# Optimization experiments

Measured on AMD Instinct MI355X. Metric: run time of the kernel, lower is better.

## Reference

```python
import jax, jax.numpy as jnp
import numpy as np

IMG, P, D, E, TOPK, H = 224, 14, 512, 10, 2, 8
NP = (IMG // P) ** 2  # 256 patches
PD = P * P            # 196
HID = 256             # expert hidden (hardcoded in source)


def _moe_layer(x, Wip, bip, Wqkv, bqkv, Wo, bo, Wg, bg, W1, b1, W2, b2):
    # input projection (input_dim == adjusted_dim == 512 here)
    h = x @ Wip + bip                                  # [b, s, d]
    b, s, d = h.shape
    hd = d // H
    # torch nn.MultiheadAttention with batch_first=False receives [b, s, d]
    # untransposed -> seq axis is the BATCH axis (l,m below), batch axis is
    # the patch axis (n). Faithfully reproduced.
    qkv = h @ Wqkv + bqkv                              # [b, s, 3d]
    q, k, v = jnp.split(qkv, 3, axis=-1)
    q = q.reshape(b, s, H, hd)
    k = k.reshape(b, s, H, hd)
    v = v.reshape(b, s, H, hd)
    scores = jnp.einsum('lnhd,mnhd->nhlm', q, k) / np.sqrt(hd)
    attn = jax.nn.softmax(scores, axis=-1)             # [s, H, b, b]
    o = jnp.einsum('nhlm,mnhd->lnhd', attn, v).reshape(b, s, d)
    o = o @ Wo + bo                                    # [b, s, d]
    # gating + top-k dispatch
    probs = jax.nn.softmax(o @ Wg + bg, axis=-1)       # [b, s, E]
    topv, topi = jax.lax.top_k(probs, TOPK)
    topv = topv / jnp.sum(topv, axis=-1, keepdims=True)
    # combine weights per (token, expert): [b, s, E]
    w = jnp.sum(jax.nn.one_hot(topi, E, dtype=o.dtype) * topv[..., None], axis=2)
    # expert MLPs (dense over experts, weighted combine == masked scatter-add)
    h1 = jax.nn.relu(jnp.einsum('bsd,edh->bseh', o, W1) + b1)   # [b, s, E, HID]
    out = jnp.einsum('bseh,eho,bse->bso', h1, W2, w) \
        + jnp.einsum('bse,eo->bso', w, b2)
    return out


def _patchify(x):
    # x: [b, 1, IMG, IMG] -> [b, NP, PD]  (unfold/unfold/permute in source)
    b = x.shape[0]
    n = IMG // P
    x = x.reshape(b, n, P, n, P)
    x = x.transpose(0, 1, 3, 2, 4)
    return x.reshape(b, n * n, PD)


def _moe_params(key, prefix):
    ks = jax.random.split(key, 12)
    g = lambda k, shape: jax.random.normal(k, shape, jnp.float32) * 0.02
    return {
        prefix + 'Wip': g(ks[0], (D, D)),   prefix + 'bip': jnp.zeros((D,), jnp.float32),
        prefix + 'Wqkv': g(ks[1], (D, 3 * D)), prefix + 'bqkv': jnp.zeros((3 * D,), jnp.float32),
        prefix + 'Wo': g(ks[2], (D, D)),    prefix + 'bo': jnp.zeros((D,), jnp.float32),
        prefix + 'Wg': g(ks[3], (D, E)),    prefix + 'bg': jnp.zeros((E,), jnp.float32),
        prefix + 'W1': g(ks[4], (E, D, HID)), prefix + 'b1': jnp.zeros((E, HID), jnp.float32),
        prefix + 'W2': g(ks[5], (E, HID, D)), prefix + 'b2': jnp.zeros((E, D), jnp.float32),
    }


def setup_inputs() -> dict:
    key = jax.random.key(0)
    ks = jax.random.split(key, 8)
    g = lambda k, shape: jax.random.normal(k, shape, jnp.float32) * 0.02
    inp = {'x': jax.random.normal(ks[0], (64, 1, IMG, IMG), jnp.float32)}
    inp['pos_emb'] = g(ks[1], (1, NP, D))
    inp['Wp'] = g(ks[2], (PD, D))
    inp['bp'] = jnp.zeros((D,), jnp.float32)
    inp.update(_moe_params(ks[3], 'm1_'))
    inp.update(_moe_params(ks[4], 'm2_'))
    inp['Wv'] = g(ks[5], (D, D))
    inp['bv'] = jnp.zeros((D,), jnp.float32)
    inp['Wc'] = g(ks[6], (D, D))
    inp['bc'] = jnp.zeros((D,), jnp.float32)
    return inp


def reference(x, pos_emb, Wp, bp,
              m1_Wip, m1_bip, m1_Wqkv, m1_bqkv, m1_Wo, m1_bo, m1_Wg, m1_bg,
              m1_W1, m1_b1, m1_W2, m1_b2,
              m2_Wip, m2_bip, m2_Wqkv, m2_bqkv, m2_Wo, m2_bo, m2_Wg, m2_bg,
              m2_W1, m2_b1, m2_W2, m2_b2,
              Wv, bv, Wc, bc):
    tok = _patchify(x) @ Wp + bp + pos_emb             # [b, NP, D]
    first = _moe_layer(tok, m1_Wip, m1_bip, m1_Wqkv, m1_bqkv, m1_Wo, m1_bo,
                       m1_Wg, m1_bg, m1_W1, m1_b1, m1_W2, m1_b2)
    first_vec = first @ Wv + bv
    second = _moe_layer(first_vec, m2_Wip, m2_bip, m2_Wqkv, m2_bqkv, m2_Wo, m2_bo,
                        m2_Wg, m2_bg, m2_W1, m2_b1, m2_W2, m2_b2)
    second_vec = second @ Wv + bv
    cls_first = first @ Wc + bc
    cls_second = second @ Wc + bc
    return (first_vec, second_vec, cls_first, cls_second)
```

## Files before the change

### kernel.cpp

```cpp
#include <hip/hip_runtime.h>
#include <cstdint>
#include <cstddef>

typedef _Float16 half_t;
typedef _Float16 h8 __attribute__((ext_vector_type(8)));
typedef float f4 __attribute__((ext_vector_type(4)));

static constexpr int TOKENS = 16384;
static constexpr int DIM    = 512;
static constexpr int NEXP   = 10;
static constexpr int EHID   = 256;
static constexpr int ECAP   = 4096;
static constexpr float LSC  = 4096.f;
static constexpr float LSCI = 1.f / 4096.f;

__device__ __forceinline__ void split_hl(float v, half_t& h, half_t& l) {
  h = (half_t)v;
  l = (half_t)((v - (float)h) * LSC);
}

__global__ __launch_bounds__(256) void k_wprep(const float* __restrict__ W,
                                               half_t* __restrict__ Ohi,
                                               half_t* __restrict__ Olo,
                                               int K, int N, int KP)
{
  __shared__ float T[32][33];
  const int z = blockIdx.z;
  W   += (size_t)z * K * N;
  Ohi += (size_t)z * N * KP;
  Olo += (size_t)z * N * KP;
  const int t = threadIdx.x;
  const int bn = blockIdx.x * 32, bk = blockIdx.y * 32;
  {
    int nl = t & 31, kq = t >> 5;
#pragma unroll
    for (int i = 0; i < 4; ++i) {
      int kl = kq + i * 8;
      int k = bk + kl;
      T[kl][nl] = (k < K) ? W[(size_t)k * N + bn + nl] : 0.f;
    }
  }
  __syncthreads();
  {
    int kl = t & 31, nq = t >> 5;
#pragma unroll
    for (int i = 0; i < 4; ++i) {
      int nl = nq + i * 8;
      half_t h, l; split_hl(T[kl][nl], h, l);
      size_t o = (size_t)(bn + nl) * KP + bk + kl;
      Ohi[o] = h; Olo[o] = l;
    }
  }
}

__global__ __launch_bounds__(256) void k_patchify(const float* __restrict__ x,
                                                  half_t* __restrict__ Phi,
                                                  half_t* __restrict__ Plo)
{
  int gid = blockIdx.x * 256 + threadIdx.x;
  if (gid >= TOKENS * 224) return;
  int tk = gid / 224, p = gid - tk * 224;
  float v = 0.f;
  if (p < 196) {
    int b = tk >> 8, n = tk & 255;
    int ni = n >> 4, nj = n & 15;
    int pi = p / 14, pj = p - pi * 14;
    v = x[(size_t)b * 50176 + (size_t)(ni * 14 + pi) * 224 + (nj * 14 + pj)];
  }
  half_t h, l; split_hl(v, h, l);
  Phi[gid] = h; Plo[gid] = l;
}

template <int EPI, bool QKVMAP>
__global__ __launch_bounds__(256) void k_mgemm(
    const half_t* __restrict__ Ahi, const half_t* __restrict__ Alo,
    const half_t* __restrict__ Bhi, const half_t* __restrict__ Blo,
    const float* __restrict__ bias, const float* __restrict__ pos,
    float* __restrict__ Cf, half_t* __restrict__ Chi, half_t* __restrict__ Clo,
    int K, int Cld, int qkvg)
{
  __shared__ half_t Ah[128][40], Al[128][40], Bh[64][40], Bl[64][40];
  const int tid = threadIdx.x;
  const int row0 = blockIdx.x * 128;
  const int by = blockIdx.y;
  const int col0 = by * 64;
  int brow0;
  if (QKVMAP) {
    int part = by >> 1;
    brow0 = part * 512 + qkvg * 128 + (by & 1) * 64;
  } else {
    brow0 = col0;
  }
  const int lane = tid & 63, wid = tid >> 6;
  const int wm = wid & 1, wn = wid >> 1;
  const int l16 = lane & 15, lq = lane >> 4;
  f4 acc1[4][2], acc2[4][2];
#pragma unroll
  for (int a = 0; a < 4; ++a)
#pragma unroll
    for (int b = 0; b < 2; ++b) {
      acc1[a][b] = {0.f, 0.f, 0.f, 0.f};
      acc2[a][b] = {0.f, 0.f, 0.f, 0.f};
    }
  const int sr = tid >> 2;
  const int sc = (tid & 3) << 3;
  for (int k0 = 0; k0 < K; k0 += 32) {
#pragma unroll
    for (int hf = 0; hf < 2; ++hf) {
      int r = sr + hf * 64;
      const size_t ga = (size_t)(row0 + r) * K + k0 + sc;
      *(uint4*)&Ah[r][sc] = *(const uint4*)&Ahi[ga];
      *(uint4*)&Al[r][sc] = *(const uint4*)&Alo[ga];
    }
    {
      const size_t gb = (size_t)(brow0 + sr) * K + k0 + sc;
      *(uint4*)&Bh[sr][sc] = *(const uint4*)&Bhi[gb];
      *(uint4*)&Bl[sr][sc] = *(const uint4*)&Blo[gb];
    }
    __syncthreads();
    h8 ah[4], al[4], bh[2], bl[2];
#pragma unroll
    for (int mt = 0; mt < 4; ++mt) {
      int r = wm * 64 + mt * 16 + l16;
      ah[mt] = *(const h8*)&Ah[r][lq * 8];
      al[mt] = *(const h8*)&Al[r][lq * 8];
    }
#pragma unroll
    for (int nt = 0; nt < 2; ++nt) {
      int r = wn * 32 + nt * 16 + l16;
      bh[nt] = *(const h8*)&Bh[r][lq * 8];
      bl[nt] = *(const h8*)&Bl[r][lq * 8];
    }
#pragma unroll
    for (int mt = 0; mt < 4; ++mt)
#pragma unroll
      for (int nt = 0; nt < 2; ++nt) {
        acc1[mt][nt] = __builtin_amdgcn_mfma_f32_16x16x32_f16(ah[mt], bh[nt], acc1[mt][nt], 0, 0, 0);
        acc2[mt][nt] = __builtin_amdgcn_mfma_f32_16x16x32_f16(ah[mt], bl[nt], acc2[mt][nt], 0, 0, 0);
        acc2[mt][nt] = __builtin_amdgcn_mfma_f32_16x16x32_f16(al[mt], bh[nt], acc2[mt][nt], 0, 0, 0);
      }
    __syncthreads();
  }
#pragma unroll
  for (int mt = 0; mt < 4; ++mt) {
#pragma unroll
    for (int nt = 0; nt < 2; ++nt) {
      const int col  = col0 + wn * 32 + nt * 16 + l16;
      const int bcol = brow0 + wn * 32 + nt * 16 + l16;
      const float bv = bias[bcol];
#pragma unroll
      for (int r = 0; r < 4; ++r) {
        const int row = row0 + wm * 64 + mt * 16 + lq * 4 + r;
        float v = acc1[mt][nt][r] + acc2[mt][nt][r] * LSCI + bv;
        if (EPI == 0) v += pos[(size_t)(row & 255) * 512 + col];
        const size_t ci = (size_t)row * Cld + col;
        if (EPI == 2 || EPI == 3) Cf[ci] = v;
        if (EPI == 0 || EPI == 1 || EPI == 3) {
          half_t h, l; split_hl(v, h, l);
          Chi[ci] = h; Clo[ci] = l;
        }
      }
    }
  }
}

__global__ __launch_bounds__(256) void k_attn2(const float* __restrict__ qkv2,
                                               half_t* __restrict__ oHi,
                                               half_t* __restrict__ oLo, int g)
{
  __shared__ float Qs[64][68];
  __shared__ float Ks[64][68];
  __shared__ float Vs[64][68];
  const int n = blockIdx.x;
  const int hp = blockIdx.y;
  const int tid = threadIdx.x;
  const int l = tid >> 2, q = tid & 3;
  {
    const float* rowp = qkv2 + (size_t)(l * 256 + n) * 384 + hp * 64;
#pragma unroll
    for (int i = 0; i < 4; ++i) {
      int c = q * 16 + i * 4;
      *(float4*)&Qs[l][c] = *(const float4*)(rowp + c);
      *(float4*)&Ks[l][c] = *(const float4*)(rowp + 128 + c);
      *(float4*)&Vs[l][c] = *(const float4*)(rowp + 256 + c);
    }
  }
  __syncthreads();
  float s[16];
#pragma unroll
  for (int j = 0; j < 16; ++j) {
    int m = (j << 2) + q;
    float a = 0.f;
#pragma unroll
    for (int k4 = 0; k4 < 16; ++k4) {
      float4 qa = *(const float4*)&Qs[l][k4 * 4];
      float4 kb = *(const float4*)&Ks[m][k4 * 4];
      a = fmaf(qa.x, kb.x, a); a = fmaf(qa.y, kb.y, a);
      a = fmaf(qa.z, kb.z, a); a = fmaf(qa.w, kb.w, a);
    }
    s[j] = a * 0.125f;
  }
  float mx = s[0];
#pragma unroll
  for (int j = 1; j < 16; ++j) mx = fmaxf(mx, s[j]);
  mx = fmaxf(mx, __shfl_xor(mx, 1));
  mx = fmaxf(mx, __shfl_xor(mx, 2));
  float sum = 0.f;
#pragma unroll
  for (int j = 0; j < 16; ++j) { s[j] = expf(s[j] - mx); sum += s[j]; }
  sum += __shfl_xor(sum, 1);
  sum += __shfl_xor(sum, 2);
  float inv = 1.f / sum;
  __syncthreads();
#pragma unroll
  for (int j = 0; j < 16; ++j) Qs[l][(j << 2) + q] = s[j] * inv;
  __syncthreads();
  float av[16] = {};
  for (int m = 0; m < 64; ++m) {
    float p = Qs[l][m];
#pragma unroll
    for (int i = 0; i < 4; ++i) {
      float4 v4 = *(const float4*)&Vs[m][q * 16 + i * 4];
      av[i * 4 + 0] = fmaf(p, v4.x, av[i * 4 + 0]);
      av[i * 4 + 1] = fmaf(p, v4.y, av[i * 4 + 1]);
      av[i * 4 + 2] = fmaf(p, v4.z, av[i * 4 + 2]);
      av[i * 4 + 3] = fmaf(p, v4.w, av[i * 4 + 3]);
    }
  }
  const int h = g * 2 + hp;
  const size_t base = (size_t)(l * 256 + n) * 512 + h * 64 + q * 16;
  h8 hv0, hv1, lv0, lv1;
#pragma unroll
  for (int i = 0; i < 8; ++i) { half_t hh, ll; split_hl(av[i], hh, ll); hv0[i] = hh; lv0[i] = ll; }
#pragma unroll
  for (int i = 0; i < 8; ++i) { half_t hh, ll; split_hl(av[8 + i], hh, ll); hv1[i] = hh; lv1[i] = ll; }
  *(h8*)&oHi[base] = hv0; *(h8*)&oHi[base + 8] = hv1;
  *(h8*)&oLo[base] = lv0; *(h8*)&oLo[base + 8] = lv1;
}

__global__ __launch_bounds__(256) void k_gate(const float* __restrict__ o2,
                                              const float* __restrict__ Wg,
                                              const float* __restrict__ bg,
                                              int2* __restrict__ tok_e,
                                              float2* __restrict__ tok_w)
{
  const int wave = threadIdx.x >> 6;
  const int lane = threadIdx.x & 63;
  const int t = blockIdx.x * 4 + wave;
  const float* xr = o2 + (size_t)t * DIM;
  float acc[NEXP];
#pragma unroll
  for (int e = 0; e < NEXP; ++e) acc[e] = 0.f;
#pragma unroll
  for (int i = 0; i < 8; ++i) {
    int d = i * 64 + lane;
    float xv = xr[d];
    const float* wr = Wg + (size_t)d * NEXP;
#pragma unroll
    for (int e = 0; e < NEXP; ++e) acc[e] = fmaf(xv, wr[e], acc[e]);
  }
#pragma unroll
  for (int e = 0; e < NEXP; ++e) {
    float v = acc[e];
    v += __shfl_xor(v, 32); v += __shfl_xor(v, 16); v += __shfl_xor(v, 8);
    v += __shfl_xor(v, 4);  v += __shfl_xor(v, 2);  v += __shfl_xor(v, 1);
    acc[e] = v;
  }
  if (lane == 0) {
    float p[NEXP];
    float mx = -1e30f;
#pragma unroll
    for (int e = 0; e < NEXP; ++e) { p[e] = acc[e] + bg[e]; mx = fmaxf(mx, p[e]); }
#pragma unroll
    for (int e = 0; e < NEXP; ++e) p[e] = expf(p[e] - mx);
    int i0 = 0;
#pragma unroll
    for (int e = 1; e < NEXP; ++e) if (p[e] > p[i0]) i0 = e;
    int i1 = (i0 == 0) ? 1 : 0;
#pragma unroll
    for (int e = 0; e < NEXP; ++e)
      if (e != i0 && e != i1 && p[e] > p[i1]) i1 = e;
    float wsum = p[i0] + p[i1];
    tok_e[t] = make_int2(i0, i1);
    tok_w[t] = make_float2(p[i0] / wsum, p[i1] / wsum);
  }
}

__global__ __launch_bounds__(256) void k_scatter(const int2* __restrict__ tok_e,
                                                 const float2* __restrict__ tok_w,
                                                 int* __restrict__ counts,
                                                 int* __restrict__ lt,
                                                 float* __restrict__ lw)
{
  __shared__ int lcnt[32];
  __shared__ int lbase[32];
  const int tid = threadIdx.x;
  if (tid < 32) lcnt[tid] = 0;
  __syncthreads();
  const int t = blockIdx.x * 256 + tid;
  int2 e = tok_e[t];
  float2 w = tok_w[t];
  int s0 = atomicAdd(&lcnt[e.x], 1);
  int s1 = atomicAdd(&lcnt[16 + e.y], 1);
  __syncthreads();
  if (tid < 32) lbase[tid] = atomicAdd(&counts[tid], lcnt[tid]);
  __syncthreads();
  int i0 = lbase[e.x] + s0;
  int i1 = lbase[16 + e.y] + s1;
  if (i0 < ECAP) { int p = e.x * ECAP + i0;            lt[p] = t; lw[p] = w.x; }
  if (i1 < ECAP) { int p = (10 + e.y) * ECAP + i1;     lt[p] = t; lw[p] = w.y; }
}

template <int MODE>
__global__ __launch_bounds__(256) void k_mexpert(
    const float* __restrict__ Af32,
    const half_t* __restrict__ BhiAll, const half_t* __restrict__ BloAll,
    const float* __restrict__ biasAll,
    const int* __restrict__ counts, const int* __restrict__ lt,
    const float* __restrict__ lw,
    float* __restrict__ Hout, half_t* __restrict__ Dhi, half_t* __restrict__ Dlo,
    int K, int N)
{
  const int z = blockIdx.z;
  int slot, e;
  if (MODE == 0) { slot = z / 10; e = z - slot * 10; }
  else           { slot = MODE - 1; e = z; }
  const int cnt = counts[slot * 16 + e];
  const int i0 = blockIdx.x * 64;
  if (i0 >= cnt) return;
  const int col0 = blockIdx.y * 64;
  __shared__ half_t Ah[64][40], Al[64][40], Bh[64][40], Bl[64][40];
  __shared__ int rows[64];
  __shared__ float wts[64];
  const int tid = threadIdx.x;
  if (tid < 64) {
    int i = i0 + tid;
    rows[tid] = (i < cnt) ? lt[(slot * 10 + e) * ECAP + i] : -1;
    wts[tid]  = (i < cnt) ? lw[(slot * 10 + e) * ECAP + i] : 0.f;
  }
  __syncthreads();
  const half_t* Bhi = BhiAll + (size_t)e * K * N;
  const half_t* Blo = BloAll + (size_t)e * K * N;
  const int lane = tid & 63, wid = tid >> 6;
  const int wm = wid & 1, wn = wid >> 1;
  const int l16 = lane & 15, lq = lane >> 4;
  f4 acc1[2][2], acc2[2][2];
#pragma unroll
  for (int a = 0; a < 2; ++a)
#pragma unroll
    for (int b = 0; b < 2; ++b) {
      acc1[a][b] = {0.f, 0.f, 0.f, 0.f};
      acc2[a][b] = {0.f, 0.f, 0.f, 0.f};
    }
  const int sr = tid >> 2;
  const int sc = (tid & 3) << 3;
  for (int k0 = 0; k0 < K; k0 += 32) {
    {
      int trow = rows[sr];
      float4 v0 = make_float4(0.f, 0.f, 0.f, 0.f), v1 = v0;
      if (trow >= 0) {
        size_t ar = (MODE == 0) ? (size_t)trow : (size_t)(trow * 2 + slot);
        const float* ap = Af32 + ar * K + k0 + sc;
        v0 = *(const float4*)ap;
        v1 = *(const float4*)(ap + 4);
      }
      h8 hh, ll;
      float vv[8] = {v0.x, v0.y, v0.z, v0.w, v1.x, v1.y, v1.z, v1.w};
#pragma unroll
      for (int i = 0; i < 8; ++i) { half_t a, b; split_hl(vv[i], a, b); hh[i] = a; ll[i] = b; }
      *(h8*)&Ah[sr][sc] = hh;
      *(h8*)&Al[sr][sc] = ll;
    }
    {
      const size_t gb = (size_t)(col0 + sr) * K + k0 + sc;
      *(uint4*)&Bh[sr][sc] = *(const uint4*)&Bhi[gb];
      *(uint4*)&Bl[sr][sc] = *(const uint4*)&Blo[gb];
    }
    __syncthreads();
    h8 ah[2], al[2], bh[2], bl[2];
#pragma unroll
    for (int mt = 0; mt < 2; ++mt) {
      int r = wm * 32 + mt * 16 + l16;
      ah[mt] = *(const h8*)&Ah[r][lq * 8];
      al[mt] = *(const h8*)&Al[r][lq * 8];
    }
#pragma unroll
    for (int nt = 0; nt < 2; ++nt) {
      int r = wn * 32 + nt * 16 + l16;
      bh[nt] = *(const h8*)&Bh[r][lq * 8];
      bl[nt] = *(const h8*)&Bl[r][lq * 8];
    }
#pragma unroll
    for (int mt = 0; mt < 2; ++mt)
#pragma unroll
      for (int nt = 0; nt < 2; ++nt) {
        acc1[mt][nt] = __builtin_amdgcn_mfma_f32_16x16x32_f16(ah[mt], bh[nt], acc1[mt][nt], 0, 0, 0);
        acc2[mt][nt] = __builtin_amdgcn_mfma_f32_16x16x32_f16(ah[mt], bl[nt], acc2[mt][nt], 0, 0, 0);
        acc2[mt][nt] = __builtin_amdgcn_mfma_f32_16x16x32_f16(al[mt], bh[nt], acc2[mt][nt], 0, 0, 0);
      }
    __syncthreads();
  }
#pragma unroll
  for (int mt = 0; mt < 2; ++mt) {
#pragma unroll
    for (int nt = 0; nt < 2; ++nt) {
      const int col = col0 + wn * 32 + nt * 16 + l16;
      const float bv = biasAll[(size_t)e * N + col];
#pragma unroll
      for (int r = 0; r < 4; ++r) {
        const int ridx = wm * 32 + mt * 16 + lq * 4 + r;
        const int trow = rows[ridx];
        if (trow < 0) continue;
        float v = acc1[mt][nt][r] + acc2[mt][nt][r] * LSCI;
        if (MODE == 0) {
          float o = fmaxf(v + bv, 0.f);
          Hout[(size_t)(trow * 2 + slot) * N + col] = o;
        } else {
          float o = wts[ridx] * (v + bv);
          const size_t di = (size_t)trow * N + col;
          if (MODE == 2) o += (float)Dhi[di] + (float)Dlo[di] * LSCI;
          half_t h, l; split_hl(o, h, l);
          Dhi[di] = h; Dlo[di] = l;
        }
      }
    }
  }
}

__global__ void k_zero(int* counts)
{
  if (threadIdx.x < 32) counts[threadIdx.x] = 0;
}

extern "C" void kernel_launch(void* const* d_in, const int* in_sizes, int n_in,
                              void* d_out, int out_size, void* d_ws, size_t ws_size,
                              hipStream_t stream)
{
  const float* x   = (const float*)d_in[0];
  const float* pos = (const float*)d_in[1];
  const float* Wp  = (const float*)d_in[2];
  const float* bp  = (const float*)d_in[3];
  const float* w1p[12];
  const float* w2p[12];
  for (int i = 0; i < 12; ++i) {
    w1p[i] = (const float*)d_in[4 + i];
    w2p[i] = (const float*)d_in[16 + i];
  }
  const float* Wv = (const float*)d_in[28];
  const float* bv = (const float*)d_in[29];
  const float* Wc = (const float*)d_in[30];
  const float* bc = (const float*)d_in[31];

  const size_t MiB = 1ull << 20;
  char* wsb = (char*)d_ws;

  half_t* wbase = (half_t*)wsb;
  size_t woff = 0;
  auto walloc = [&](size_t n) { half_t* p = wbase + woff; woff += n; return p; };
  half_t* wpT_hi = walloc(512 * 224);
  half_t* wpT_lo = walloc(512 * 224);
  struct LayerW {
    half_t *wip_h, *wip_l, *wqkv_h, *wqkv_l, *wo_h, *wo_l, *w1_h, *w1_l, *w2_h, *w2_l;
  } lw_[2];
  for (int L = 0; L < 2; ++L) {
    lw_[L].wip_h  = walloc(512 * 512);       lw_[L].wip_l  = walloc(512 * 512);
    lw_[L].wqkv_h = walloc(1536 * 512);      lw_[L].wqkv_l = walloc(1536 * 512);
    lw_[L].wo_h   = walloc(512 * 512);       lw_[L].wo_l   = walloc(512 * 512);
    lw_[L].w1_h   = walloc(10 * 256 * 512);  lw_[L].w1_l   = walloc(10 * 256 * 512);
    lw_[L].w2_h   = walloc(10 * 512 * 256);  lw_[L].w2_l   = walloc(10 * 512 * 256);
  }
  half_t* wvT_hi = walloc(512 * 512);
  half_t* wvT_lo = walloc(512 * 512);
  half_t* wcT_hi = walloc(512 * 512);
  half_t* wcT_lo = walloc(512 * 512);

  char* sm = wsb + 33 * MiB;
  int*    counts = (int*)sm;
  int*    lt     = (int*)(sm + 1024);
  float*  lwt    = (float*)(sm + 1024 + 327680);
  int2*   tok_e  = (int2*)(sm + 1024 + 655360);
  float2* tok_w  = (float2*)(sm + 1024 + 655360 + 131072);

  char* RA = wsb + 34 * MiB;
  char* RB = wsb + 66 * MiB;
  char* RC = wsb + 98 * MiB;
  char* RD = wsb + 122 * MiB;
  half_t* tokHi = (half_t*)RA;          half_t* tokLo = (half_t*)(RA + 16 * MiB);
  float*  H1    = (float*)RA;
  half_t* fvHi  = (half_t*)RA;          half_t* fvLo  = (half_t*)(RA + 16 * MiB);
  half_t* hHi   = (half_t*)RB;          half_t* hLo   = (half_t*)(RB + 16 * MiB);
  float*  o2    = (float*)RB;
  half_t* PHi   = (half_t*)RC;          half_t* PLo   = (half_t*)(RC + 7 * MiB);
  float*  qkv2  = (float*)RC;
  half_t* atHi  = (half_t*)RD;          half_t* atLo  = (half_t*)(RD + 16 * MiB);
  half_t* dstHi = (half_t*)RD;          half_t* dstLo = (half_t*)(RD + 16 * MiB);

  float* out0 = (float*)d_out;
  float* out1 = out0 + 8388608;
  float* out2 = out0 + 16777216;
  float* out3 = out0 + 25165824;

  k_wprep<<<dim3(16, 7, 1),  dim3(256), 0, stream>>>(Wp, wpT_hi, wpT_lo, 196, 512, 224);
  for (int L = 0; L < 2; ++L) {
    const float* const* w = (L == 0) ? w1p : w2p;
    k_wprep<<<dim3(16, 16, 1),  dim3(256), 0, stream>>>(w[0], lw_[L].wip_h,  lw_[L].wip_l,  512, 512, 512);
    k_wprep<<<dim3(48, 16, 1),  dim3(256), 0, stream>>>(w[2], lw_[L].wqkv_h, lw_[L].wqkv_l, 512, 1536, 512);
    k_wprep<<<dim3(16, 16, 1),  dim3(256), 0, stream>>>(w[4], lw_[L].wo_h,   lw_[L].wo_l,   512, 512, 512);
    k_wprep<<<dim3(8, 16, 10),  dim3(256), 0, stream>>>(w[8], lw_[L].w1_h,   lw_[L].w1_l,   512, 256, 512);
    k_wprep<<<dim3(16, 8, 10),  dim3(256), 0, stream>>>(w[10], lw_[L].w2_h,  lw_[L].w2_l,   256, 512, 256);
  }
  k_wprep<<<dim3(16, 16, 1), dim3(256), 0, stream>>>(Wv, wvT_hi, wvT_lo, 512, 512, 512);
  k_wprep<<<dim3(16, 16, 1), dim3(256), 0, stream>>>(Wc, wcT_hi, wcT_lo, 512, 512, 512);

  k_patchify<<<dim3(14336), dim3(256), 0, stream>>>(x, PHi, PLo);
  k_mgemm<0, false><<<dim3(128, 8), dim3(256), 0, stream>>>(
      PHi, PLo, wpT_hi, wpT_lo, bp, pos, nullptr, tokHi, tokLo, 224, 512, 0);

  auto moe = [&](int L, const half_t* inHi, const half_t* inLo) {
    const LayerW& W = lw_[L];
    const float* const* w = (L == 0) ? w1p : w2p;
    k_zero<<<dim3(1), dim3(64), 0, stream>>>(counts);
    k_mgemm<1, false><<<dim3(128, 8), dim3(256), 0, stream>>>(
        inHi, inLo, W.wip_h, W.wip_l, w[1], nullptr, nullptr, hHi, hLo, 512, 512, 0);
    for (int g = 0; g < 4; ++g) {
      k_mgemm<2, true><<<dim3(128, 6), dim3(256), 0, stream>>>(
          hHi, hLo, W.wqkv_h, W.wqkv_l, w[3], nullptr, qkv2, nullptr, nullptr, 512, 384, g);
      k_attn2<<<dim3(256, 2), dim3(256), 0, stream>>>(qkv2, atHi, atLo, g);
    }
    k_mgemm<2, false><<<dim3(128, 8), dim3(256), 0, stream>>>(
        atHi, atLo, W.wo_h, W.wo_l, w[5], nullptr, o2, nullptr, nullptr, 512, 512, 0);
    k_gate<<<dim3(4096), dim3(256), 0, stream>>>(o2, w[6], w[7], tok_e, tok_w);
    k_scatter<<<dim3(64), dim3(256), 0, stream>>>(tok_e, tok_w, counts, lt, lwt);
    k_mexpert<0><<<dim3(64, 4, 20), dim3(256), 0, stream>>>(
        o2, W.w1_h, W.w1_l, w[9], counts, lt, lwt, H1, nullptr, nullptr, 512, 256);
    k_mexpert<1><<<dim3(64, 8, 10), dim3(256), 0, stream>>>(
        H1, W.w2_h, W.w2_l, w[11], counts, lt, lwt, nullptr, dstHi, dstLo, 256, 512);
    k_mexpert<2><<<dim3(64, 8, 10), dim3(256), 0, stream>>>(
        H1, W.w2_h, W.w2_l, w[11], counts, lt, lwt, nullptr, dstHi, dstLo, 256, 512);
  };

  moe(0, tokHi, tokLo);
  k_mgemm<3, false><<<dim3(128, 8), dim3(256), 0, stream>>>(
      dstHi, dstLo, wvT_hi, wvT_lo, bv, nullptr, out0, fvHi, fvLo, 512, 512, 0);
  k_mgemm<2, false><<<dim3(128, 8), dim3(256), 0, stream>>>(
      dstHi, dstLo, wcT_hi, wcT_lo, bc, nullptr, out2, nullptr, nullptr, 512, 512, 0);
  moe(1, fvHi, fvLo);
  k_mgemm<2, false><<<dim3(128, 8), dim3(256), 0, stream>>>(
      dstHi, dstLo, wvT_hi, wvT_lo, bv, nullptr, out1, nullptr, nullptr, 512, 512, 0);
  k_mgemm<2, false><<<dim3(128, 8), dim3(256), 0, stream>>>(
      dstHi, dstLo, wcT_hi, wcT_lo, bc, nullptr, out3, nullptr, nullptr, 512, 512, 0);
}
```

Before: 1.399 ms.

## Widen GEMM tiles to 128x128 and compute full QKV in one pass

New measurement: 1.542 ms. 1.1x slower.

```diff
diff --git a/kernel.cpp b/kernel.cpp
--- a/kernel.cpp
+++ b/kernel.cpp
@@ -71,83 +71,69 @@
   Phi[gid] = h; Plo[gid] = l;
 }
 
-template <int EPI, bool QKVMAP>
+template <int EPI>
 __global__ __launch_bounds__(256) void k_mgemm(
     const half_t* __restrict__ Ahi, const half_t* __restrict__ Alo,
     const half_t* __restrict__ Bhi, const half_t* __restrict__ Blo,
     const float* __restrict__ bias, const float* __restrict__ pos,
     float* __restrict__ Cf, half_t* __restrict__ Chi, half_t* __restrict__ Clo,
-    int K, int Cld, int qkvg)
-{
-  __shared__ half_t Ah[128][40], Al[128][40], Bh[64][40], Bl[64][40];
+    int K, int Cld)
+{
+  __shared__ half_t Ah[128][40], Al[128][40], Bh[128][40], Bl[128][40];
   const int tid = threadIdx.x;
   const int row0 = blockIdx.x * 128;
-  const int by = blockIdx.y;
-  const int col0 = by * 64;
-  int brow0;
-  if (QKVMAP) {
-    int part = by >> 1;
-    brow0 = part * 512 + qkvg * 128 + (by & 1) * 64;
-  } else {
-    brow0 = col0;
-  }
+  const int col0 = blockIdx.y * 128;
   const int lane = tid & 63, wid = tid >> 6;
   const int wm = wid & 1, wn = wid >> 1;
   const int l16 = lane & 15, lq = lane >> 4;
-  f4 acc1[4][2], acc2[4][2];
+  f4 acc1[4][4], acc2[4][4];
 #pragma unroll
   for (int a = 0; a < 4; ++a)
 #pragma unroll
-    for (int b = 0; b < 2; ++b) {
+    for (int b = 0; b < 4; ++b) {
       acc1[a][b] = {0.f, 0.f, 0.f, 0.f};
       acc2[a][b] = {0.f, 0.f, 0.f, 0.f};
     }
-  const int sr = tid >> 2;
-  const int sc = (tid & 3) << 3;
   for (int k0 = 0; k0 < K; k0 += 32) {
 #pragma unroll
-    for (int hf = 0; hf < 2; ++hf) {
-      int r = sr + hf * 64;
-      const size_t ga = (size_t)(row0 + r) * K + k0 + sc;
-      *(uint4*)&Ah[r][sc] = *(const uint4*)&Ahi[ga];
-      *(uint4*)&Al[r][sc] = *(const uint4*)&Alo[ga];
-    }
-    {
-      const size_t gb = (size_t)(brow0 + sr) * K + k0 + sc;
-      *(uint4*)&Bh[sr][sc] = *(const uint4*)&Bhi[gb];
-      *(uint4*)&Bl[sr][sc] = *(const uint4*)&Blo[gb];
+    for (int i = 0; i < 2; ++i) {
+      int lin = tid + i * 256;
+      int r = lin >> 2, kc = (lin & 3) << 3;
+      const size_t ga = (size_t)(row0 + r) * K + k0 + kc;
+      *(uint4*)&Ah[r][kc] = *(const uint4*)&Ahi[ga];
+      *(uint4*)&Al[r][kc] = *(const uint4*)&Alo[ga];
+      const size_t gb = (size_t)(col0 + r) * K + k0 + kc;
+      *(uint4*)&Bh[r][kc] = *(const uint4*)&Bhi[gb];
+      *(uint4*)&Bl[r][kc] = *(const uint4*)&Blo[gb];
     }
     __syncthreads();
-    h8 ah[4], al[4], bh[2], bl[2];
+    h8 ah[4], al2[4];
 #pragma unroll
     for (int mt = 0; mt < 4; ++mt) {
       int r = wm * 64 + mt * 16 + l16;
-      ah[mt] = *(const h8*)&Ah[r][lq * 8];
-      al[mt] = *(const h8*)&Al[r][lq * 8];
-    }
-#pragma unroll
-    for (int nt = 0; nt < 2; ++nt) {
-      int r = wn * 32 + nt * 16 + l16;
-      bh[nt] = *(const h8*)&Bh[r][lq * 8];
-      bl[nt] = *(const h8*)&Bl[r][lq * 8];
-    }
-#pragma unroll
-    for (int mt = 0; mt < 4; ++mt)
-#pragma unroll
-      for (int nt = 0; nt < 2; ++nt) {
-        acc1[mt][nt] = __builtin_amdgcn_mfma_f32_16x16x32_f16(ah[mt], bh[nt], acc1[mt][nt], 0, 0, 0);
-        acc2[mt][nt] = __builtin_amdgcn_mfma_f32_16x16x32_f16(ah[mt], bl[nt], acc2[mt][nt], 0, 0, 0);
-        acc2[mt][nt] = __builtin_amdgcn_mfma_f32_16x16x32_f16(al[mt], bh[nt], acc2[mt][nt], 0, 0, 0);
+      ah[mt]  = *(const h8*)&Ah[r][lq * 8];
+      al2[mt] = *(const h8*)&Al[r][lq * 8];
+    }
+#pragma unroll
+    for (int nt = 0; nt < 4; ++nt) {
+      int rb = wn * 64 + nt * 16 + l16;
+      h8 bh = *(const h8*)&Bh[rb][lq * 8];
+      h8 bl = *(const h8*)&Bl[rb][lq * 8];
+#pragma unroll
+      for (int mt = 0; mt < 4; ++mt) {
+        acc1[mt][nt] = __builtin_amdgcn_mfma_f32_16x16x32_f16(ah[mt], bh, acc1[mt][nt], 0, 0, 0);
+        acc2[mt][nt] = __builtin_amdgcn_mfma_f32_16x16x32_f16(ah[mt], bl, acc2[mt][nt], 0, 0, 0);
+        acc2[mt][nt] = __builtin_amdgcn_mfma_f32_16x16x32_f16(al2[mt], bh, acc2[mt][nt], 0, 0, 0);
       }
+    }
     __syncthreads();
   }
 #pragma unroll
   for (int mt = 0; mt < 4; ++mt) {
 #pragma unroll
-    for (int nt = 0; nt < 2; ++nt) {
-      const int col  = col0 + wn * 32 + nt * 16 + l16;
-      const int bcol = brow0 + wn * 32 + nt * 16 + l16;
-      const float bv = bias[bcol];
+    for (int nt = 0; nt < 4; ++nt) {
+      const int col = col0 + wn * 64 + nt * 16 + l16;
+      const float bv = bias[col];
 #pragma unroll
       for (int r = 0; r < 4; ++r) {
         const int row = row0 + wm * 64 + mt * 16 + lq * 4 + r;
@@ -164,25 +150,25 @@
   }
 }
 
-__global__ __launch_bounds__(256) void k_attn2(const float* __restrict__ qkv2,
-                                               half_t* __restrict__ oHi,
-                                               half_t* __restrict__ oLo, int g)
+__global__ __launch_bounds__(256) void k_attn(const float* __restrict__ qkv,
+                                              half_t* __restrict__ oHi,
+                                              half_t* __restrict__ oLo)
 {
   __shared__ float Qs[64][68];
   __shared__ float Ks[64][68];
   __shared__ float Vs[64][68];
   const int n = blockIdx.x;
-  const int hp = blockIdx.y;
+  const int h = blockIdx.y;
   const int tid = threadIdx.x;
   const int l = tid >> 2, q = tid & 3;
   {
-    const float* rowp = qkv2 + (size_t)(l * 256 + n) * 384 + hp * 64;
+    const float* rowp = qkv + (size_t)(l * 256 + n) * 1536 + h * 64;
 #pragma unroll
     for (int i = 0; i < 4; ++i) {
       int c = q * 16 + i * 4;
       *(float4*)&Qs[l][c] = *(const float4*)(rowp + c);
-      *(float4*)&Ks[l][c] = *(const float4*)(rowp + 128 + c);
-      *(float4*)&Vs[l][c] = *(const float4*)(rowp + 256 + c);
+      *(float4*)&Ks[l][c] = *(const float4*)(rowp + 512 + c);
+      *(float4*)&Vs[l][c] = *(const float4*)(rowp + 1024 + c);
     }
   }
   __syncthreads();
@@ -227,7 +213,6 @@
       av[i * 4 + 3] = fmaf(p, v4.w, av[i * 4 + 3]);
     }
   }
-  const int h = g * 2 + hp;
   const size_t base = (size_t)(l * 256 + n) * 512 + h * 64 + q * 16;
   h8 hv0, hv1, lv0, lv1;
 #pragma unroll
@@ -377,12 +362,12 @@
       *(uint4*)&Bl[sr][sc] = *(const uint4*)&Blo[gb];
     }
     __syncthreads();
-    h8 ah[2], al[2], bh[2], bl[2];
+    h8 ah[2], al2[2], bh[2], bl[2];
 #pragma unroll
     for (int mt = 0; mt < 2; ++mt) {
       int r = wm * 32 + mt * 16 + l16;
-      ah[mt] = *(const h8*)&Ah[r][lq * 8];
-      al[mt] = *(const h8*)&Al[r][lq * 8];
+      ah[mt]  = *(const h8*)&Ah[r][lq * 8];
+      al2[mt] = *(const h8*)&Al[r][lq * 8];
     }
 #pragma unroll
     for (int nt = 0; nt < 2; ++nt) {
@@ -396,7 +381,7 @@
       for (int nt = 0; nt < 2; ++nt) {
         acc1[mt][nt] = __builtin_amdgcn_mfma_f32_16x16x32_f16(ah[mt], bh[nt], acc1[mt][nt], 0, 0, 0);
         acc2[mt][nt] = __builtin_amdgcn_mfma_f32_16x16x32_f16(ah[mt], bl[nt], acc2[mt][nt], 0, 0, 0);
-        acc2[mt][nt] = __builtin_amdgcn_mfma_f32_16x16x32_f16(al[mt], bh[nt], acc2[mt][nt], 0, 0, 0);
+        acc2[mt][nt] = __builtin_amdgcn_mfma_f32_16x16x32_f16(al2[mt], bh[nt], acc2[mt][nt], 0, 0, 0);
       }
     __syncthreads();
   }
@@ -483,17 +468,17 @@
 
   char* RA = wsb + 34 * MiB;
   char* RB = wsb + 66 * MiB;
-  char* RC = wsb + 98 * MiB;
-  char* RD = wsb + 122 * MiB;
+  char* RD = wsb + 98 * MiB;
+  char* RQ = wsb + 130 * MiB;
   half_t* tokHi = (half_t*)RA;          half_t* tokLo = (half_t*)(RA + 16 * MiB);
   float*  H1    = (float*)RA;
   half_t* fvHi  = (half_t*)RA;          half_t* fvLo  = (half_t*)(RA + 16 * MiB);
   half_t* hHi   = (half_t*)RB;          half_t* hLo   = (half_t*)(RB + 16 * MiB);
   float*  o2    = (float*)RB;
-  half_t* PHi   = (half_t*)RC;          half_t* PLo   = (half_t*)(RC + 7 * MiB);
-  float*  qkv2  = (float*)RC;
   half_t* atHi  = (half_t*)RD;          half_t* atLo  = (half_t*)(RD + 16 * MiB);
   half_t* dstHi = (half_t*)RD;          half_t* dstLo = (half_t*)(RD + 16 * MiB);
+  half_t* PHi   = (half_t*)RQ;          half_t* PLo   = (half_t*)(RQ + 8 * MiB);
+  float*  qkvf  = (float*)RQ;
 
   float* out0 = (float*)d_out;
   float* out1 = out0 + 8388608;
@@ -513,22 +498,20 @@
   k_wprep<<<dim3(16, 16, 1), dim3(256), 0, stream>>>(Wc, wcT_hi, wcT_lo, 512, 512, 512);
 
   k_patchify<<<dim3(14336), dim3(256), 0, stream>>>(x, PHi, PLo);
-  k_mgemm<0, false><<<dim3(128, 8), dim3(256), 0, stream>>>(
-      PHi, PLo, wpT_hi, wpT_lo, bp, pos, nullptr, tokHi, tokLo, 224, 512, 0);
+  k_mgemm<0><<<dim3(128, 4), dim3(256), 0, stream>>>(
+      PHi, PLo, wpT_hi, wpT_lo, bp, pos, nullptr, tokHi, tokLo, 224, 512);
 
   auto moe = [&](int L, const half_t* inHi, const half_t* inLo) {
     const LayerW& W = lw_[L];
     const float* const* w = (L == 0) ? w1p : w2p;
     k_zero<<<dim3(1), dim3(64), 0, stream>>>(counts);
-    k_mgemm<1, false><<<dim3(128, 8), dim3(256), 0, stream>>>(
-        inHi, inLo, W.wip_h, W.wip_l, w[1], nullptr, nullptr, hHi, hLo, 512, 512, 0);
-    for (int g = 0; g < 4; ++g) {
-      k_mgemm<2, true><<<dim3(128, 6), dim3(256), 0, stream>>>(
-          hHi, hLo, W.wqkv_h, W.wqkv_l, w[3], nullptr, qkv2, nullptr, nullptr, 512, 384, g);
-      k_attn2<<<dim3(256, 2), dim3(256), 0, stream>>>(qkv2, atHi, atLo, g);
-    }
-    k_mgemm<2, false><<<dim3(128, 8), dim3(256), 0, stream>>>(
-        atHi, atLo, W.wo_h, W.wo_l, w[5], nullptr, o2, nullptr, nullptr, 512, 512, 0);
+    k_mgemm<1><<<dim3(128, 4), dim3(256), 0, stream>>>(
+        inHi, inLo, W.wip_h, W.wip_l, w[1], nullptr, nullptr, hHi, hLo, 512, 512);
+    k_mgemm<2><<<dim3(128, 12), dim3(256), 0, stream>>>(
+        hHi, hLo, W.wqkv_h, W.wqkv_l, w[3], nullptr, qkvf, nullptr, nullptr, 512, 1536);
+    k_attn<<<dim3(256, 8), dim3(256), 0, stream>>>(qkvf, atHi, atLo);
+    k_mgemm<2><<<dim3(128, 4), dim3(256), 0, stream>>>(
+        atHi, atLo, W.wo_h, W.wo_l, w[5], nullptr, o2, nullptr, nullptr, 512, 512);
     k_gate<<<dim3(4096), dim3(256), 0, stream>>>(o2, w[6], w[7], tok_e, tok_w);
     k_scatter<<<dim3(64), dim3(256), 0, stream>>>(tok_e, tok_w, counts, lt, lwt);
     k_mexpert<0><<<dim3(64, 4, 20), dim3(256), 0, stream>>>(
@@ -540,13 +523,13 @@
   };
 
   moe(0, tokHi, tokLo);
-  k_mgemm<3, false><<<dim3(128, 8), dim3(256), 0, stream>>>(
-      dstHi, dstLo, wvT_hi, wvT_lo, bv, nullptr, out0, fvHi, fvLo, 512, 512, 0);
-  k_mgemm<2, false><<<dim3(128, 8), dim3(256), 0, stream>>>(
-      dstHi, dstLo, wcT_hi, wcT_lo, bc, nullptr, out2, nullptr, nullptr, 512, 512, 0);
+  k_mgemm<3><<<dim3(128, 4), dim3(256), 0, stream>>>(
+      dstHi, dstLo, wvT_hi, wvT_lo, bv, nullptr, out0, fvHi, fvLo, 512, 512);
+  k_mgemm<2><<<dim3(128, 4), dim3(256), 0, stream>>>(
+      dstHi, dstLo, wcT_hi, wcT_lo, bc, nullptr, out2, nullptr, nullptr, 512, 512);
   moe(1, fvHi, fvLo);
-  k_mgemm<2, false><<<dim3(128, 8), dim3(256), 0, stream>>>(
-      dstHi, dstLo, wvT_hi, wvT_lo, bv, nullptr, out1, nullptr, nullptr, 512, 512, 0);
-  k_mgemm<2, false><<<dim3(128, 8), dim3(256), 0, stream>>>(
-      dstHi, dstLo, wcT_hi, wcT_lo, bc, nullptr, out3, nullptr, nullptr, 512, 512, 0);
-}
+  k_mgemm<2><<<dim3(128, 4), dim3(256), 0, stream>>>(
+      dstHi, dstLo, wvT_hi, wvT_lo, bv, nullptr, out1, nullptr, nullptr, 512, 512);
+  k_mgemm<2><<<dim3(128, 4), dim3(256), 0, stream>>>(
+      dstHi, dstLo, wcT_hi, wcT_lo, bc, nullptr, out3, nullptr, nullptr, 512, 512);
+}
```
